# Kernel tuning notes

Hardware: AMD Instinct MI355X
Metric: run time of the kernel (lower is better)

The kernel has to match this reference:

```python
import jax, jax.numpy as jnp
import numpy as np


def setup_inputs() -> dict:
    key = jax.random.key(0)
    kW, kH, kT = jax.random.split(key, 3)
    N, rank, M = 1024, 8, 4096
    W = jax.random.normal(kW, (N, rank), dtype=jnp.float32)
    H = jax.random.normal(kH, (rank, M), dtype=jnp.float32)
    tau = jax.random.normal(kT, (N, rank), dtype=jnp.float32)
    return {"W": W, "H": H, "tau": tau}


def reference(W, H, tau):
    # W: [N, rank] float, H: [rank, M] float, tau: [N, rank] float
    M = H.shape[1]
    Nf = M // 2 + 1
    # FFT of nonneg-constrained H, keep first Nf bins, rebuild full Hermitian spectrum
    Hf = jnp.fft.fft(jax.nn.softplus(H), axis=1)[:, :Nf]            # [rank, Nf]
    Hf_rev = Hf[:, 1:Nf - 1][:, ::-1]                               # [rank, M - Nf]
    Hft = jnp.concatenate([Hf, jnp.conj(Hf_rev)], axis=1)           # [rank, M]
    f = jnp.arange(M, dtype=jnp.float32) / M                        # [M]
    # phase shift per (sample, component, freq): omega = exp(-i 2 pi tau f)
    omega = jnp.exp((-2j * jnp.pi) * (tau[:, :, None] * f))         # [N, rank, M] complex64
    Wp = jax.nn.softplus(W).astype(omega.dtype)                     # [N, rank]
    # fused: V[N,M] = sum_d softplus(W)[N,d] * omega[N,d,M] * Hft[d,M]
    V = jnp.einsum('Nd,NdM,dM->NM', Wp, omega, Hft)
    return V
```

## Files before the change

### kernel.cpp

```cpp
#include <hip/hip_runtime.h>
#include <math.h>

#define N_ROWS 1024
#define RANK   8
#define M_COLS 4096

#define R_ROWS   2
#define T_PTS    2
#define M_STRIDE 1024

__device__ float2 g_Hft[RANK * M_COLS];
__device__ float4 g_Tab4[N_ROWS * RANK];
__device__ float2 g_Tab2[N_ROWS * RANK];

__device__ __forceinline__ float softplus_f(float x) {
    float t = __expf(x);
    float r = 0.69314718056f * __log2f(1.0f + t);
    return (x > 20.0f) ? x : r;
}
__device__ __forceinline__ float sin_rev(float x) { return __builtin_amdgcn_sinf(x); }
__device__ __forceinline__ float cos_rev(float x) { return __builtin_amdgcn_cosf(x); }
__device__ __forceinline__ float fract_f(float x) { return __builtin_amdgcn_fractf(x); }
__device__ __forceinline__ float rfl(float x) {
    return __int_as_float(__builtin_amdgcn_readfirstlane(__float_as_int(x)));
}

__global__ void fft_fused(const float* __restrict__ H,
                          const float* __restrict__ W,
                          const float* __restrict__ tau) {
    __shared__ float  sHs[M_COLS];
    __shared__ float2 sY [4 * 64];
    __shared__ float2 sP [512];

    const int tid = threadIdx.x;
    const int b   = blockIdx.x;
    const int d   = b >> 4;
    const int m0b = (b & 15) << 2;

    if (b < 16) {
        int t = b * 512 + tid;
        float w  = softplus_f(W[t]);
        float tv = tau[t];
        float rv = fract_f(tv * ((float)M_STRIDE / (float)M_COLS));
        float4 t4;
        t4.x = cos_rev(rv);
        t4.y = sin_rev(rv);
        float rc = fract_f(-tv);
        t4.z = w * cos_rev(rc);
        t4.w = w * sin_rev(rc);
        g_Tab4[t] = t4;
        g_Tab2[t] = make_float2(w, tv);
    }

    const float4* Hrow4 = (const float4*)(H + d * M_COLS);
    #pragma unroll
    for (int p = 0; p < 2; ++p) {
        int i = p * 512 + tid;
        float4 h4 = Hrow4[i];
        sHs[i*4+0] = softplus_f(h4.x);
        sHs[i*4+1] = softplus_f(h4.y);
        sHs[i*4+2] = softplus_f(h4.z);
        sHs[i*4+3] = softplus_f(h4.w);
    }
    __syncthreads();

    {
        int k0   = tid & 63;
        int m0j  = (tid >> 6) & 3;
        int half = tid >> 8;
        int m0   = m0b + m0j;
        float mrev = (float)m0 * (1.0f / 64.0f);
        float rr =  cos_rev(mrev);
        float ri = -sin_rev(mrev);
        float twr = ((half & m0) & 1) ? -1.0f : 1.0f;
        float twi = 0.0f;
        float ar = 0.0f, ai = 0.0f;
        int base = half << 5;
        #pragma unroll
        for (int k = 0; k < 32; ++k) {
            float v = sHs[((base + k) << 6) + k0];
            ar = fmaf(v, twr, ar);
            ai = fmaf(v, twi, ai);
            float nr = fmaf(twr, rr, -(twi * ri));
            twi      = fmaf(twr, ri,   twi * rr);
            twr = nr;
        }
        sP[tid] = make_float2(ar, ai);
    }
    __syncthreads();
    if (tid < 256) {
        float2 a = sP[tid], c = sP[256 + tid];
        sY[tid] = make_float2(a.x + c.x, a.y + c.y);
    }
    __syncthreads();

    {
        int m1   = tid & 63;
        int m0j  = (tid >> 6) & 3;
        int half = tid >> 8;
        int m    = (m1 << 6) + m0b + m0j;
        float mrev = (float)m * (1.0f / 4096.0f);
        float rr =  cos_rev(mrev);
        float ri = -sin_rev(mrev);
        float irev = (float)((m * (half << 5)) & 4095) * (1.0f / 4096.0f);
        float twr =  cos_rev(irev);
        float twi = -sin_rev(irev);
        float ar = 0.0f, ai = 0.0f;
        int base = half << 5;
        #pragma unroll
        for (int k = 0; k < 32; ++k) {
            float2 y = sY[(m0j << 6) + base + k];
            ar = fmaf(y.x, twr, fmaf(-y.y, twi, ar));
            ai = fmaf(y.x, twi, fmaf( y.y, twr, ai));
            float nr = fmaf(twr, rr, -(twi * ri));
            twi      = fmaf(twr, ri,   twi * rr);
            twr = nr;
        }
        sP[tid] = make_float2(ar, ai);
    }
    __syncthreads();
    if (tid < 256) {
        int m1 = tid & 63, m0j = tid >> 6;
        float2 a = sP[tid], c = sP[256 + tid];
        int m = (m1 << 6) + m0b + m0j;
        g_Hft[d * M_COLS + m] = make_float2(a.x + c.x, a.y + c.y);
    }
}

__global__ void shiftnmf_main(float* __restrict__ out) {
    int tid = threadIdx.x;
    int m0  = blockIdx.x * 256 + tid;
    int n0  = blockIdx.y * R_ROWS;

    float fm0 = (float)(1 + m0) * (1.0f / (float)M_COLS);

    float accm[R_ROWS][T_PTS];
    float accx[R_ROWS][T_PTS];
    #pragma unroll
    for (int r = 0; r < R_ROWS; ++r)
        #pragma unroll
        for (int j = 0; j < T_PTS; ++j) { accm[r][j] = 0.0f; accx[r][j] = 0.0f; }

    #pragma unroll
    for (int d = 0; d < RANK; ++d) {
        float ur[R_ROWS], ui[R_ROWS];
        float vr[R_ROWS], vi[R_ROWS];
        float ws[R_ROWS], wcr[R_ROWS], wci[R_ROWS];
        #pragma unroll
        for (int r = 0; r < R_ROWS; ++r) {
            int nd = (n0 + r) * RANK + d;
            float4 t4 = g_Tab4[nd];
            vr[r]  = rfl(t4.x);  vi[r]  = rfl(t4.y);
            wcr[r] = rfl(t4.z);  wci[r] = rfl(t4.w);
            ws[r]  = rfl(g_Tab2[nd].x);
            float tv = rfl(g_Tab2[nd].y);
            float r0 = fract_f(tv * fm0);
            ur[r] = cos_rev(r0);
            ui[r] = sin_rev(r0);
        }

        const float2* hp = g_Hft + d * M_COLS + 1 + m0;
        #pragma unroll
        for (int j = 0; j < T_PTS; ++j) {
            float2 h = hp[j * M_STRIDE];
            #pragma unroll
            for (int r = 0; r < R_ROWS; ++r) {
                float t1v = ui[r] * h.y;
                float zr = fmaf(ur[r], h.x, t1v);
                float t2v = ui[r] * h.x;
                float zi = fmaf(ur[r], h.y, -t2v);
                accm[r][j] = fmaf(ws[r],  zr, accm[r][j]);
                accx[r][j] = fmaf(wcr[r], zr, fmaf(wci[r], zi, accx[r][j]));
                if (j < T_PTS - 1) {
                    float nr = fmaf(ur[r], vr[r], -(ui[r] * vi[r]));
                    ui[r]    = fmaf(ur[r], vi[r],   ui[r] * vr[r]);
                    ur[r]    = nr;
                }
            }
        }
    }

    #pragma unroll
    for (int r = 0; r < R_ROWS; ++r) {
        float* op = out + (n0 + r) * M_COLS;
        #pragma unroll
        for (int j = 0; j < T_PTS; ++j)
            op[1 + m0 + j * M_STRIDE] = accm[r][j];
        #pragma unroll
        for (int j = 0; j < T_PTS; ++j)
            op[4095 - m0 - j * M_STRIDE] = accx[r][j];
    }

    if (blockIdx.x == 0 && tid == 0) {
        #pragma unroll
        for (int r = 0; r < R_ROWS; ++r) {
            int n = n0 + r;
            float a = 0.0f;
            #pragma unroll
            for (int d = 0; d < RANK; ++d)
                a = fmaf(g_Tab2[n * RANK + d].x, g_Hft[d * M_COLS].x, a);
            out[n * M_COLS] = a;
        }
    }
}

extern "C" void kernel_launch(void* const* d_in, const int* in_sizes, int n_in,
                              void* d_out, int out_size, void* d_ws, size_t ws_size,
                              hipStream_t stream) {
    const float* W   = (const float*)d_in[0];
    const float* H   = (const float*)d_in[1];
    const float* tau = (const float*)d_in[2];

    fft_fused<<<dim3(128), dim3(512), 0, stream>>>(H, W, tau);

    dim3 grid(M_COLS / 2 / (256 * T_PTS), N_ROWS / R_ROWS);
    shiftnmf_main<<<grid, dim3(256), 0, stream>>>((float*)d_out);
}
```

Baseline: 18.84 us.

## Factor per-column phase into precomputed coarse and fine twiddle tables

```diff
diff --git a/kernel.cpp b/kernel.cpp
--- a/kernel.cpp
+++ b/kernel.cpp
@@ -12,6 +12,8 @@
 __device__ float2 g_Hft[RANK * M_COLS];
 __device__ float4 g_Tab4[N_ROWS * RANK];
 __device__ float2 g_Tab2[N_ROWS * RANK];
+__device__ float2 g_T1[N_ROWS * RANK * 64];
+__device__ float2 g_T2[N_ROWS * RANK * 16];
 
 __device__ __forceinline__ float softplus_f(float x) {
     float t = __expf(x);
@@ -28,12 +30,32 @@
 __global__ void fft_fused(const float* __restrict__ H,
                           const float* __restrict__ W,
                           const float* __restrict__ tau) {
+    const int tid = threadIdx.x;
+    const int b   = blockIdx.x;
+
+    if (b >= 128) {
+        if (b < 1152) {
+            int idx = (b - 128) * 512 + tid;
+            int nd  = idx >> 6;
+            int l   = idx & 63;
+            float tv  = tau[nd];
+            float rev = fract_f(tv * ((float)l * (1.0f / (float)M_COLS)));
+            g_T1[idx] = make_float2(cos_rev(rev), sin_rev(rev));
+        } else {
+            int idx = (b - 1152) * 512 + tid;
+            int nd  = idx >> 4;
+            int qq  = idx & 15;
+            float tv  = tau[nd];
+            float rev = fract_f(tv * ((float)(1 + 64 * qq) * (1.0f / (float)M_COLS)));
+            g_T2[idx] = make_float2(cos_rev(rev), sin_rev(rev));
+        }
+        return;
+    }
+
     __shared__ float  sHs[M_COLS];
     __shared__ float2 sY [4 * 64];
     __shared__ float2 sP [512];
 
-    const int tid = threadIdx.x;
-    const int b   = blockIdx.x;
     const int d   = b >> 4;
     const int m0b = (b & 15) << 2;
 
@@ -128,11 +150,24 @@
 }
 
 __global__ void shiftnmf_main(float* __restrict__ out) {
-    int tid = threadIdx.x;
-    int m0  = blockIdx.x * 256 + tid;
-    int n0  = blockIdx.y * R_ROWS;
-
-    float fm0 = (float)(1 + m0) * (1.0f / (float)M_COLS);
+    __shared__ float2 sT1[2 * RANK * 64];
+    __shared__ float2 sT2[2 * RANK * 16];
+
+    const int tid = threadIdx.x;
+    const int bx  = blockIdx.x;
+    const int m0  = bx * 256 + tid;
+    const int n0  = blockIdx.y * R_ROWS;
+    const int l   = tid & 63;
+    const int qq  = (bx << 2) + (tid >> 6);
+
+    {
+        const float2* src = g_T1 + n0 * (RANK * 64);
+        #pragma unroll
+        for (int p = 0; p < 4; ++p)
+            sT1[p * 256 + tid] = src[p * 256 + tid];
+        sT2[tid] = g_T2[n0 * (RANK * 16) + tid];
+    }
+    __syncthreads();
 
     float accm[R_ROWS][T_PTS];
     float accx[R_ROWS][T_PTS];
@@ -153,10 +188,11 @@
             vr[r]  = rfl(t4.x);  vi[r]  = rfl(t4.y);
             wcr[r] = rfl(t4.z);  wci[r] = rfl(t4.w);
             ws[r]  = rfl(g_Tab2[nd].x);
-            float tv = rfl(g_Tab2[nd].y);
-            float r0 = fract_f(tv * fm0);
-            ur[r] = cos_rev(r0);
-            ui[r] = sin_rev(r0);
+            float2 u0 = sT2[(r * RANK + d) * 16 + qq];
+            float u0r = rfl(u0.x), u0i = rfl(u0.y);
+            float2 t1 = sT1[(r * RANK + d) * 64 + l];
+            ur[r] = fmaf(u0r, t1.x, -(u0i * t1.y));
+            ui[r] = fmaf(u0r, t1.y,   u0i * t1.x);
         }
 
         const float2* hp = g_Hft + d * M_COLS + 1 + m0;
@@ -191,7 +227,7 @@
             op[4095 - m0 - j * M_STRIDE] = accx[r][j];
     }
 
-    if (blockIdx.x == 0 && tid == 0) {
+    if (bx == 0 && tid == 0) {
         #pragma unroll
         for (int r = 0; r < R_ROWS; ++r) {
             int n = n0 + r;
@@ -211,7 +247,7 @@
     const float* H   = (const float*)d_in[1];
     const float* tau = (const float*)d_in[2];
 
-    fft_fused<<<dim3(128), dim3(512), 0, stream>>>(H, W, tau);
+    fft_fused<<<dim3(1408), dim3(512), 0, stream>>>(H, W, tau);
 
     dim3 grid(M_COLS / 2 / (256 * T_PTS), N_ROWS / R_ROWS);
     shiftnmf_main<<<grid, dim3(256), 0, stream>>>((float*)d_out);
```

Result: slower. 24.40 us (+29.5%).
